# Optimization experiments

Hardware: AMD Instinct MI355X
Metric: run time of the kernel (lower is better)

The kernel has to match this reference:

```python
import jax, jax.numpy as jnp
import numpy as np

B, N, K, T, H = 4, 1024, 100, 2, 64
NFEAT = 96  # ntypes * m1 * m2 = 2 * 12 * 4


def setup_inputs() -> dict:
    key = jax.random.key(0)
    ks = jax.random.split(key, 8)
    feat = jax.random.normal(ks[0], (B, N, NFEAT), jnp.float32)
    dfeat = jax.random.normal(ks[1], (B, N, K, NFEAT, 3), jnp.float32) * 0.1
    ImageDR = jax.random.uniform(ks[2], (B, N, K, 4), jnp.float32)
    # 1-based neighbor indices; 0 marks an empty (padded) neighbor slot
    list_neigh_alltype = jax.random.randint(ks[3], (B, N, K), 0, N + 1).astype(jnp.int32)
    Imagetype_map = jnp.sort(jax.random.randint(ks[4], (N,), 0, T)).astype(jnp.int32)
    # per-type FittingNet params: 96 -> 64 -> 64 (resnet w/ resnet_dt) -> 1
    W1 = jax.random.normal(ks[5], (T, NFEAT, H), jnp.float32) * (1.0 / np.sqrt(NFEAT))
    b1 = jnp.zeros((T, H), jnp.float32)
    W2 = jax.random.normal(ks[6], (T, H, H), jnp.float32) * (1.0 / np.sqrt(H))
    b2 = jnp.zeros((T, H), jnp.float32)
    rdt = jnp.full((T, H), 0.1, jnp.float32)  # resnet_dt timestep params
    Wout = jax.random.normal(ks[7], (T, H), jnp.float32) * (1.0 / np.sqrt(H))
    bout = jnp.array([-3.2, -5.1], jnp.float32)  # per-type energy shift
    return dict(feat=feat, dfeat=dfeat, ImageDR=ImageDR,
                list_neigh_alltype=list_neigh_alltype, Imagetype_map=Imagetype_map,
                W1=W1, b1=b1, W2=W2, b2=b2, rdt=rdt, Wout=Wout, bout=bout, nghost=0)


def _fitting_Ei(feat, Imagetype_map, W1, b1, W2, b2, rdt, Wout, bout):
    # Evaluate every per-type fitting net on all atoms, then select by atom type.
    h1 = jnp.tanh(jnp.einsum('bnf,tfh->tbnh', feat, W1) + b1[:, None, None, :])
    h2 = h1 + rdt[:, None, None, :] * jnp.tanh(
        jnp.einsum('tbnh,thg->tbng', h1, W2) + b2[:, None, None, :])
    e = jnp.einsum('tbnh,th->tbn', h2, Wout) + bout[:, None, None]  # (T,B,N)
    sel = Imagetype_map.astype(jnp.int32)[None, :, None]            # (1,N,1)
    Ei = jnp.take_along_axis(e.transpose(1, 2, 0), sel, axis=2)[..., 0]  # (B,N)
    return Ei


def reference(feat, dfeat, ImageDR, list_neigh_alltype, Imagetype_map,
              W1, b1, W2, b2, rdt, Wout, bout, nghost):
    # Ei and dE/dfeat (the torch code uses autograd.grad on Ei wrt feat)
    Ei, vjp_fn = jax.vjp(
        lambda f: _fitting_Ei(f, Imagetype_map, W1, b1, W2, b2, rdt, Wout, bout), feat)
    Etot = Ei.sum(axis=1)                                    # (B,)
    dE = vjp_fn(jnp.ones_like(Ei))[0]                        # (B,N,NFEAT)
    # dE_dfeat[b,i,k,:] = sum_f dE[b,i,f] * dfeat[b,i,k,f,:]
    dE_dfeat = jnp.einsum('bnf,bnkfx->bnkx', dE, dfeat)      # (B,N,K,3)
    valid = (list_neigh_alltype > 0).astype(dE_dfeat.dtype)[..., None]
    pair_f = dE_dfeat * valid
    # force buffer sized natoms + nghost + 1; slot 0 absorbs padded neighbors
    Fbuf = jnp.zeros((B, N + 1 + nghost, 3), dE_dfeat.dtype)
    bidx = jnp.arange(B)[:, None, None]
    Fbuf = Fbuf.at[bidx, list_neigh_alltype].add(pair_f)     # scatter to neighbors
    Fbuf = Fbuf.at[:, 1:N + 1, :].add(-pair_f.sum(axis=2))   # center-atom reaction
    Force = Fbuf[:, 1:N + 1, :]                              # (B,N,3)
    rij = ImageDR[..., 1:4]                                  # (B,N,K,3)
    Virial = -jnp.einsum('bnkx,bnky->bxy', rij, pair_f).reshape(B, 9)
    return Etot, Ei, Force, Virial
```

## Files before the change

### kernel.cpp

```cpp
#include <hip/hip_runtime.h>

#define BB 4
#define NN 1024
#define KK 100
#define TT 2
#define HH 64
#define FF 96

#define OFF_EI   4
#define OFF_F    (4 + BB*NN)
#define OFF_VIR  (4 + BB*NN + BB*NN*3)
#define OUT_TOT  (4 + BB*NN + BB*NN*3 + BB*9)

__device__ __forceinline__ float wave_sum(float v) {
    #pragma unroll
    for (int off = 32; off > 0; off >>= 1)
        v += __shfl_xor(v, off, 64);
    return v;
}

__global__ __launch_bounds__(256) void zero_kernel(float* __restrict__ out) {
    int i = blockIdx.x * blockDim.x + threadIdx.x;
    for (int idx = i; idx < OUT_TOT; idx += gridDim.x * blockDim.x)
        out[idx] = 0.f;
}

__global__ __launch_bounds__(64) void mlp_kernel(
    const float* __restrict__ feat, const int* __restrict__ tmap,
    const float* __restrict__ W1, const float* __restrict__ b1,
    const float* __restrict__ W2, const float* __restrict__ b2,
    const float* __restrict__ rdt, const float* __restrict__ Wout,
    const float* __restrict__ bout,
    float* __restrict__ out, float* __restrict__ dE)
{
    const int row  = blockIdx.x;
    const int b    = row / NN;
    const int n    = row - b * NN;
    const int lane = threadIdx.x;
    const int t    = tmap[n];

    __shared__ float sfeat[FF];
    __shared__ float sh1[HH];
    __shared__ float sdz2[HH];
    __shared__ float sdz1[HH];

    const float* frow = feat + (size_t)row * FF;
    sfeat[lane] = frow[lane];
    if (lane < FF - HH) sfeat[HH + lane] = frow[HH + lane];
    __syncthreads();

    const float* W1t = W1 + (size_t)t * FF * HH;
    const float* W2t = W2 + (size_t)t * HH * HH;

    float z1 = b1[t * HH + lane];
    #pragma unroll 8
    for (int f = 0; f < FF; ++f) z1 = fmaf(sfeat[f], W1t[f * HH + lane], z1);
    float h1 = tanhf(z1);
    sh1[lane] = h1;
    __syncthreads();

    float z2 = b2[t * HH + lane];
    #pragma unroll 8
    for (int h = 0; h < HH; ++h) z2 = fmaf(sh1[h], W2t[h * HH + lane], z2);
    float u  = tanhf(z2);
    float r  = rdt[t * HH + lane];
    float wo = Wout[t * HH + lane];
    float h2 = h1 + r * u;

    float e = wave_sum(h2 * wo);

    float dz2 = r * wo * (1.f - u * u);
    sdz2[lane] = dz2;
    __syncthreads();

    float dh1 = wo;
    #pragma unroll 8
    for (int g = 0; g < HH; ++g) dh1 = fmaf(sdz2[g], W2t[lane * HH + g], dh1);
    float dz1 = dh1 * (1.f - h1 * h1);
    sdz1[lane] = dz1;
    __syncthreads();

    float* dErow = dE + (size_t)row * FF;
    {
        float acc = 0.f;
        #pragma unroll 8
        for (int h = 0; h < HH; ++h) acc = fmaf(sdz1[h], W1t[lane * HH + h], acc);
        dErow[lane] = acc;
    }
    if (lane < FF - HH) {
        const int f = HH + lane;
        float acc = 0.f;
        #pragma unroll 8
        for (int h = 0; h < HH; ++h) acc = fmaf(sdz1[h], W1t[f * HH + h], acc);
        dErow[f] = acc;
    }

    if (lane == 0) {
        float Ei = e + bout[t];
        out[OFF_EI + row] = Ei;
        atomicAdd(&out[b], Ei);
    }
}

__global__ __launch_bounds__(256) void pair_kernel(
    const float* __restrict__ dfeat, const float* __restrict__ ImageDR,
    const int* __restrict__ neigh, const float* __restrict__ dE,
    float* __restrict__ out)
{
    const int row  = blockIdx.x;
    const int b    = row / NN;
    const int tid  = threadIdx.x;
    const int wave = tid >> 6;
    const int lane = tid & 63;

    __shared__ float sdE[FF];
    __shared__ float swf[4][3];
    __shared__ float svir[4][9];

    if (tid < FF) sdE[tid] = dE[(size_t)row * FF + tid];
    __syncthreads();

    float sacc0 = 0.f, sacc1 = 0.f, sacc2 = 0.f;
    float vacc  = 0.f;
    const int vx = lane / 3, vy = lane - 3 * (lane / 3);

    const float* drbase = ImageDR + (size_t)row * KK * 4;
    const int*   nb     = neigh   + (size_t)row * KK;

    for (int k = wave; k < KK; k += 4) {
        const float* dfp = dfeat + ((size_t)row * KK + k) * (FF * 3);
        float a0, a1, a2;
        {
            const int f = lane;
            const float w = sdE[f];
            a0 = dfp[f * 3 + 0] * w;
            a1 = dfp[f * 3 + 1] * w;
            a2 = dfp[f * 3 + 2] * w;
        }
        if (lane < FF - HH) {
            const int f = HH + lane;
            const float w = sdE[f];
            a0 = fmaf(dfp[f * 3 + 0], w, a0);
            a1 = fmaf(dfp[f * 3 + 1], w, a1);
            a2 = fmaf(dfp[f * 3 + 2], w, a2);
        }
        float pf0 = wave_sum(a0);
        float pf1 = wave_sum(a1);
        float pf2 = wave_sum(a2);

        const int j = nb[k];
        if (j <= 0) { pf0 = 0.f; pf1 = 0.f; pf2 = 0.f; }

        if (j > 0 && lane < 3) {
            const float v = (lane == 0) ? pf0 : ((lane == 1) ? pf1 : pf2);
            atomicAdd(&out[OFF_F + ((size_t)b * NN + (j - 1)) * 3 + lane], v);
        }

        sacc0 -= pf0; sacc1 -= pf1; sacc2 -= pf2;

        if (lane < 9) {
            const float rx  = drbase[k * 4 + 1 + vx];
            const float pfy = (vy == 0) ? pf0 : ((vy == 1) ? pf1 : pf2);
            vacc = fmaf(-rx, pfy, vacc);
        }
    }

    if (lane < 3) swf[wave][lane] = (lane == 0) ? sacc0 : ((lane == 1) ? sacc1 : sacc2);
    if (lane < 9) svir[wave][lane] = vacc;
    __syncthreads();

    if (tid < 3) {
        const float s = swf[0][tid] + swf[1][tid] + swf[2][tid] + swf[3][tid];
        atomicAdd(&out[OFF_F + (size_t)row * 3 + tid], s);
    }
    if (tid < 9) {
        const float s = svir[0][tid] + svir[1][tid] + svir[2][tid] + svir[3][tid];
        atomicAdd(&out[OFF_VIR + b * 9 + tid], s);
    }
}

extern "C" void kernel_launch(void* const* d_in, const int* in_sizes, int n_in,
                              void* d_out, int out_size, void* d_ws, size_t ws_size,
                              hipStream_t stream) {
    const float* feat    = (const float*)d_in[0];
    const float* dfeat   = (const float*)d_in[1];
    const float* ImageDR = (const float*)d_in[2];
    const int*   neigh   = (const int*)  d_in[3];
    const int*   tmap    = (const int*)  d_in[4];
    const float* W1      = (const float*)d_in[5];
    const float* b1      = (const float*)d_in[6];
    const float* W2      = (const float*)d_in[7];
    const float* b2      = (const float*)d_in[8];
    const float* rdt     = (const float*)d_in[9];
    const float* Wout    = (const float*)d_in[10];
    const float* bout    = (const float*)d_in[11];

    float* out = (float*)d_out;
    float* dE  = (float*)d_ws;

    zero_kernel<<<64, 256, 0, stream>>>(out);
    mlp_kernel<<<BB * NN, 64, 0, stream>>>(feat, tmap, W1, b1, W2, b2, rdt, Wout, bout, out, dE);
    pair_kernel<<<BB * NN, 256, 0, stream>>>(dfeat, ImageDR, neigh, dE, out);
}
```

Baseline: 765.5 us.

## Fuse per-atom MLP backward into pair kernel and stage neighbor data in LDS

Merges the MLP forward/backward kernel into the pair-force kernel, so wave 0 of each block computes dE for its atom and hands it to the other waves through shared memory. This removes the dE round-trip through global workspace and one kernel launch. The MLP now uses cross-lane shuffles instead of LDS broadcasts. ImageDR and neighbor indices are prefetched into LDS, and the zero kernel launch is resized. The cost is that three of four waves sit idle while wave 0 runs the serial MLP before the dfeat streaming loop starts, which is partly hidden by other resident blocks.

```diff
diff --git a/kernel.cpp b/kernel.cpp
--- a/kernel.cpp
+++ b/kernel.cpp
@@ -3,14 +3,13 @@
 #define BB 4
 #define NN 1024
 #define KK 100
-#define TT 2
 #define HH 64
 #define FF 96
 
 #define OFF_EI   4
 #define OFF_F    (4 + BB*NN)
-#define OFF_VIR  (4 + BB*NN + BB*NN*3)
-#define OUT_TOT  (4 + BB*NN + BB*NN*3 + BB*9)
+#define OFF_VIR  (OFF_F + BB*NN*3)
+#define OUT_TOT  (OFF_VIR + BB*9)
 
 __device__ __forceinline__ float wave_sum(float v) {
     #pragma unroll
@@ -20,138 +19,117 @@
 }
 
 __global__ __launch_bounds__(256) void zero_kernel(float* __restrict__ out) {
-    int i = blockIdx.x * blockDim.x + threadIdx.x;
-    for (int idx = i; idx < OUT_TOT; idx += gridDim.x * blockDim.x)
-        out[idx] = 0.f;
+    int i = blockIdx.x * 256 + threadIdx.x;
+    if (i < OUT_TOT) out[i] = 0.f;
 }
 
-__global__ __launch_bounds__(64) void mlp_kernel(
+__global__ __launch_bounds__(256) void fused_kernel(
     const float* __restrict__ feat, const int* __restrict__ tmap,
     const float* __restrict__ W1, const float* __restrict__ b1,
     const float* __restrict__ W2, const float* __restrict__ b2,
     const float* __restrict__ rdt, const float* __restrict__ Wout,
     const float* __restrict__ bout,
-    float* __restrict__ out, float* __restrict__ dE)
+    const float* __restrict__ dfeat, const float* __restrict__ ImageDR,
+    const int* __restrict__ neigh, float* __restrict__ out)
 {
     const int row  = blockIdx.x;
     const int b    = row / NN;
     const int n    = row - b * NN;
-    const int lane = threadIdx.x;
-    const int t    = tmap[n];
-
-    __shared__ float sfeat[FF];
-    __shared__ float sh1[HH];
-    __shared__ float sdz2[HH];
-    __shared__ float sdz1[HH];
-
-    const float* frow = feat + (size_t)row * FF;
-    sfeat[lane] = frow[lane];
-    if (lane < FF - HH) sfeat[HH + lane] = frow[HH + lane];
-    __syncthreads();
-
-    const float* W1t = W1 + (size_t)t * FF * HH;
-    const float* W2t = W2 + (size_t)t * HH * HH;
-
-    float z1 = b1[t * HH + lane];
-    #pragma unroll 8
-    for (int f = 0; f < FF; ++f) z1 = fmaf(sfeat[f], W1t[f * HH + lane], z1);
-    float h1 = tanhf(z1);
-    sh1[lane] = h1;
-    __syncthreads();
-
-    float z2 = b2[t * HH + lane];
-    #pragma unroll 8
-    for (int h = 0; h < HH; ++h) z2 = fmaf(sh1[h], W2t[h * HH + lane], z2);
-    float u  = tanhf(z2);
-    float r  = rdt[t * HH + lane];
-    float wo = Wout[t * HH + lane];
-    float h2 = h1 + r * u;
-
-    float e = wave_sum(h2 * wo);
-
-    float dz2 = r * wo * (1.f - u * u);
-    sdz2[lane] = dz2;
-    __syncthreads();
-
-    float dh1 = wo;
-    #pragma unroll 8
-    for (int g = 0; g < HH; ++g) dh1 = fmaf(sdz2[g], W2t[lane * HH + g], dh1);
-    float dz1 = dh1 * (1.f - h1 * h1);
-    sdz1[lane] = dz1;
-    __syncthreads();
-
-    float* dErow = dE + (size_t)row * FF;
-    {
-        float acc = 0.f;
-        #pragma unroll 8
-        for (int h = 0; h < HH; ++h) acc = fmaf(sdz1[h], W1t[lane * HH + h], acc);
-        dErow[lane] = acc;
-    }
-    if (lane < FF - HH) {
-        const int f = HH + lane;
-        float acc = 0.f;
-        #pragma unroll 8
-        for (int h = 0; h < HH; ++h) acc = fmaf(sdz1[h], W1t[f * HH + h], acc);
-        dErow[f] = acc;
-    }
-
-    if (lane == 0) {
-        float Ei = e + bout[t];
-        out[OFF_EI + row] = Ei;
-        atomicAdd(&out[b], Ei);
-    }
-}
-
-__global__ __launch_bounds__(256) void pair_kernel(
-    const float* __restrict__ dfeat, const float* __restrict__ ImageDR,
-    const int* __restrict__ neigh, const float* __restrict__ dE,
-    float* __restrict__ out)
-{
-    const int row  = blockIdx.x;
-    const int b    = row / NN;
     const int tid  = threadIdx.x;
     const int wave = tid >> 6;
     const int lane = tid & 63;
 
     __shared__ float sdE[FF];
+    __shared__ float sdr[KK * 4];
+    __shared__ int   snb[KK];
     __shared__ float swf[4][3];
     __shared__ float svir[4][9];
 
-    if (tid < FF) sdE[tid] = dE[(size_t)row * FF + tid];
+    const float* drbase = ImageDR + (size_t)row * (KK * 4);
+    for (int i = tid; i < KK * 4; i += 256) sdr[i] = drbase[i];
+    if (tid < KK) snb[tid] = neigh[(size_t)row * KK + tid];
+
+    if (wave == 0) {
+        const int t = tmap[n];
+        const float* frow = feat + (size_t)row * FF;
+        const float* W1t  = W1 + (size_t)t * FF * HH;
+        const float* W2t  = W2 + (size_t)t * HH * HH;
+
+        float f0 = frow[lane];
+        float f1 = (lane < 32) ? frow[HH + lane] : 0.f;
+
+        float z1 = b1[t * HH + lane];
+        #pragma unroll 8
+        for (int f = 0; f < HH; ++f)
+            z1 = fmaf(__shfl(f0, f, 64), W1t[f * HH + lane], z1);
+        #pragma unroll 8
+        for (int f = 0; f < FF - HH; ++f)
+            z1 = fmaf(__shfl(f1, f, 64), W1t[(HH + f) * HH + lane], z1);
+        float h1 = tanhf(z1);
+
+        float z2 = b2[t * HH + lane];
+        #pragma unroll 8
+        for (int h = 0; h < HH; ++h)
+            z2 = fmaf(__shfl(h1, h, 64), W2t[h * HH + lane], z2);
+        float u  = tanhf(z2);
+        float r  = rdt[t * HH + lane];
+        float wo = Wout[t * HH + lane];
+
+        float e = wave_sum((h1 + r * u) * wo);
+
+        float dz2 = r * wo * (1.f - u * u);
+        float dh1 = wo;
+        #pragma unroll 8
+        for (int g = 0; g < HH; ++g)
+            dh1 = fmaf(__shfl(dz2, g, 64), W2t[lane * HH + g], dh1);
+        float dz1 = dh1 * (1.f - h1 * h1);
+
+        float acc0 = 0.f, acc1 = 0.f;
+        #pragma unroll 8
+        for (int h = 0; h < HH; ++h) {
+            const float d = __shfl(dz1, h, 64);
+            acc0 = fmaf(d, W1t[lane * HH + h], acc0);
+            if (lane < 32) acc1 = fmaf(d, W1t[(HH + lane) * HH + h], acc1);
+        }
+        sdE[lane] = acc0;
+        if (lane < 32) sdE[HH + lane] = acc1;
+
+        if (lane == 0) {
+            const float Ei = e + bout[t];
+            out[OFF_EI + row] = Ei;
+            atomicAdd(&out[b], Ei);
+        }
+    }
     __syncthreads();
+
+    const float w0 = sdE[lane];
+    const float w1 = (lane < 32) ? sdE[HH + lane] : 0.f;
 
     float sacc0 = 0.f, sacc1 = 0.f, sacc2 = 0.f;
     float vacc  = 0.f;
-    const int vx = lane / 3, vy = lane - 3 * (lane / 3);
+    const int vx = lane / 3, vy = lane - 3 * vx;
 
-    const float* drbase = ImageDR + (size_t)row * KK * 4;
-    const int*   nb     = neigh   + (size_t)row * KK;
+    const size_t pbase = (size_t)row * KK;
 
+    #pragma unroll 2
     for (int k = wave; k < KK; k += 4) {
-        const float* dfp = dfeat + ((size_t)row * KK + k) * (FF * 3);
-        float a0, a1, a2;
-        {
-            const int f = lane;
-            const float w = sdE[f];
-            a0 = dfp[f * 3 + 0] * w;
-            a1 = dfp[f * 3 + 1] * w;
-            a2 = dfp[f * 3 + 2] * w;
-        }
-        if (lane < FF - HH) {
-            const int f = HH + lane;
-            const float w = sdE[f];
-            a0 = fmaf(dfp[f * 3 + 0], w, a0);
-            a1 = fmaf(dfp[f * 3 + 1], w, a1);
-            a2 = fmaf(dfp[f * 3 + 2], w, a2);
+        const float* dfp = dfeat + (pbase + k) * (FF * 3);
+        float a0 = dfp[lane * 3 + 0] * w0;
+        float a1 = dfp[lane * 3 + 1] * w0;
+        float a2 = dfp[lane * 3 + 2] * w0;
+        if (lane < 32) {
+            const int m = (HH + lane) * 3;
+            a0 = fmaf(dfp[m + 0], w1, a0);
+            a1 = fmaf(dfp[m + 1], w1, a1);
+            a2 = fmaf(dfp[m + 2], w1, a2);
         }
         float pf0 = wave_sum(a0);
         float pf1 = wave_sum(a1);
         float pf2 = wave_sum(a2);
 
-        const int j = nb[k];
+        const int j = snb[k];
         if (j <= 0) { pf0 = 0.f; pf1 = 0.f; pf2 = 0.f; }
-
-        if (j > 0 && lane < 3) {
+        else if (lane < 3) {
             const float v = (lane == 0) ? pf0 : ((lane == 1) ? pf1 : pf2);
             atomicAdd(&out[OFF_F + ((size_t)b * NN + (j - 1)) * 3 + lane], v);
         }
@@ -159,24 +137,20 @@
         sacc0 -= pf0; sacc1 -= pf1; sacc2 -= pf2;
 
         if (lane < 9) {
-            const float rx  = drbase[k * 4 + 1 + vx];
+            const float rx  = sdr[k * 4 + 1 + vx];
             const float pfy = (vy == 0) ? pf0 : ((vy == 1) ? pf1 : pf2);
             vacc = fmaf(-rx, pfy, vacc);
         }
     }
 
-    if (lane < 3) swf[wave][lane] = (lane == 0) ? sacc0 : ((lane == 1) ? sacc1 : sacc2);
+    if (lane < 3) swf[wave][lane]  = (lane == 0) ? sacc0 : ((lane == 1) ? sacc1 : sacc2);
     if (lane < 9) svir[wave][lane] = vacc;
     __syncthreads();
 
-    if (tid < 3) {
-        const float s = swf[0][tid] + swf[1][tid] + swf[2][tid] + swf[3][tid];
-        atomicAdd(&out[OFF_F + (size_t)row * 3 + tid], s);
-    }
-    if (tid < 9) {
-        const float s = svir[0][tid] + svir[1][tid] + svir[2][tid] + svir[3][tid];
-        atomicAdd(&out[OFF_VIR + b * 9 + tid], s);
-    }
+    if (tid < 3) atomicAdd(&out[OFF_F + (size_t)row * 3 + tid],
+                           swf[0][tid] + swf[1][tid] + swf[2][tid] + swf[3][tid]);
+    if (tid < 9) atomicAdd(&out[OFF_VIR + b * 9 + tid],
+                           svir[0][tid] + svir[1][tid] + svir[2][tid] + svir[3][tid]);
 }
 
 extern "C" void kernel_launch(void* const* d_in, const int* in_sizes, int n_in,
@@ -196,9 +170,8 @@
     const float* bout    = (const float*)d_in[11];
 
     float* out = (float*)d_out;
-    float* dE  = (float*)d_ws;
 
-    zero_kernel<<<64, 256, 0, stream>>>(out);
-    mlp_kernel<<<BB * NN, 64, 0, stream>>>(feat, tmap, W1, b1, W2, b2, rdt, Wout, bout, out, dE);
-    pair_kernel<<<BB * NN, 256, 0, stream>>>(dfeat, ImageDR, neigh, dE, out);
+    zero_kernel<<<(OUT_TOT + 255) / 256, 256, 0, stream>>>(out);
+    fused_kernel<<<BB * NN, 256, 0, stream>>>(feat, tmap, W1, b1, W2, b2, rdt,
+                                              Wout, bout, dfeat, ImageDR, neigh, out);
 }
```

Measured after the change: 741.6 us. 3.1% less time.
